# Optimization experiments

Hardware: AMD Instinct MI355X
Metric: run time of the kernel (lower is better)

Reference implementation:

```python
import jax, jax.numpy as jnp
import numpy as np
from functools import partial

# Gate order along axis 0 of Wi/bi/Wh/bh: 0=r (input gate), 1=f (forget), 2=g (cell), 3=o (output)

def setup_inputs() -> dict:
    key = jax.random.key(0)
    ks = jax.random.split(key, 6)
    B, T, V, E, H, O = 64, 512, 32000, 256, 512, 1
    s_e, s_h = 1.0 / np.sqrt(E), 1.0 / np.sqrt(H)
    return {
        "input_words": jax.random.randint(ks[0], (B, T), 0, V, dtype=jnp.int64),
        "emb": jax.random.normal(ks[1], (V, E), dtype=jnp.float32) * 0.02,
        "Wi": jax.random.normal(ks[2], (4, H, E), dtype=jnp.float32) * s_e,
        "bi": jnp.zeros((4, H), dtype=jnp.float32),
        "Wh": jax.random.normal(ks[3], (4, H, H), dtype=jnp.float32) * s_h,
        "bh": jnp.zeros((4, H), dtype=jnp.float32),
        "Wfc": jax.random.normal(ks[4], (O, H), dtype=jnp.float32) * s_h,
        "bfc": jnp.zeros((O,), dtype=jnp.float32),
    }


def reference(input_words, emb, Wi, bi, Wh, bh, Wfc, bfc):
    B, T = input_words.shape
    H = Wh.shape[-1]
    x = emb[input_words]                     # [B, T, E]
    # Precompute input projections for all 4 gates, all timesteps: one big GEMM.
    xg = jnp.einsum('bte,ghe->tbgh', x, Wi) + bi  # [T, B, 4, H]

    def step(carry, xg_t):
        h, c = carry
        gates = xg_t + jnp.einsum('bk,ghk->bgh', h, Wh) + bh  # [B, 4, H]
        r = jax.nn.sigmoid(gates[:, 0])
        f = jax.nn.sigmoid(gates[:, 1])
        g = jnp.tanh(gates[:, 2])
        o = jax.nn.sigmoid(gates[:, 3])
        c = f * c + r * g
        h = o * jnp.tanh(c)
        return (h, c), None

    h0 = jnp.zeros((B, H), dtype=x.dtype)
    c0 = jnp.zeros((B, H), dtype=x.dtype)
    (h, c), _ = jax.lax.scan(step, (h0, c0), xg)
    out = jax.nn.sigmoid(h @ Wfc.T + bfc)    # [B, n_output]
    return (out, h)
```

## Files before the change

kernel.cpp:

```cpp
#include <hip/hip_runtime.h>
#include <hip/hip_bf16.h>

#define TB 512
#define NB 64
#define EE 256
#define HH 512
#define ND 8
#define DB 8
#define NBLK 8
#define NT 256
#define NCOLP 260
#define NPAIR 256
#define GCOLS 2048
#define SLOWOFF ((size_t)0x40000)
#define XGOFF   ((size_t)1 << 20)

typedef __bf16 bf16_t;
typedef bf16_t bf16x8 __attribute__((ext_vector_type(8)));
typedef float  f32x4  __attribute__((ext_vector_type(4)));
typedef unsigned u32;
typedef unsigned long long u64;
typedef u32 u32x4 __attribute__((ext_vector_type(4)));

__device__ __forceinline__ float sigf(float x) { return 1.0f / (1.0f + __expf(-x)); }
__device__ __forceinline__ float tanhfast(float x) {
    float xc = fminf(fmaxf(x, -15.0f), 15.0f);
    float e  = __expf(2.0f * xc);
    return (e - 1.0f) / (e + 1.0f);
}
__device__ __forceinline__ u32 bfbits(float f) {
    bf16_t h = (bf16_t)f;
    return (u32)__builtin_bit_cast(unsigned short, h);
}
__device__ __forceinline__ bf16x8 cvt8(float4 a, float4 b) {
    bf16x8 v;
    v[0]=(bf16_t)a.x; v[1]=(bf16_t)a.y; v[2]=(bf16_t)a.z; v[3]=(bf16_t)a.w;
    v[4]=(bf16_t)b.x; v[5]=(bf16_t)b.y; v[6]=(bf16_t)b.z; v[7]=(bf16_t)b.w;
    return v;
}
__device__ __forceinline__ f32x4 cvtxg(u64 v) {
    f32x4 r;
    r[0] = __uint_as_float((u32)( v        & 0xFFFFu) << 16);
    r[1] = __uint_as_float((u32)((v >> 16) & 0xFFFFu) << 16);
    r[2] = __uint_as_float((u32)((v >> 32) & 0xFFFFu) << 16);
    r[3] = __uint_as_float((u32)((v >> 48) & 0xFFFFu) << 16);
    return r;
}

__device__ __forceinline__ void bar_lds() {
    __builtin_amdgcn_sched_barrier(0);
    asm volatile("s_waitcnt lgkmcnt(0)" ::: "memory");
    __builtin_amdgcn_s_barrier();
    __builtin_amdgcn_sched_barrier(0);
}

__device__ __forceinline__ void poll8_dual(const u64* fsrc, const u64* ssrc,
                                           u32 tag, u64 (&pk)[4]) {
    u64 fa = (u64)fsrc;
    int it = 0;
    for (;;) {
        u32x4 q0, q1, q2, q3;
        asm volatile(
            "global_load_dwordx4 %0, %4, off sc0\n\t"
            "global_load_dwordx4 %1, %4, off offset:16 sc0\n\t"
            "global_load_dwordx4 %2, %4, off offset:32 sc0\n\t"
            "global_load_dwordx4 %3, %4, off offset:48 sc0\n\t"
            "s_waitcnt vmcnt(0)"
            : "=&v"(q0), "=&v"(q1), "=&v"(q2), "=&v"(q3)
            : "v"(fa)
            : "memory");
        if (q0[1]==tag && q0[3]==tag && q1[1]==tag && q1[3]==tag &&
            q2[1]==tag && q2[3]==tag && q3[1]==tag && q3[3]==tag) {
            pk[0] = (u64)q0[0] | ((u64)q0[2] << 32);
            pk[1] = (u64)q1[0] | ((u64)q1[2] << 32);
            pk[2] = (u64)q2[0] | ((u64)q2[2] << 32);
            pk[3] = (u64)q3[0] | ((u64)q3[2] << 32);
            return;
        }
        if (((++it) & 7) == 0) {
            u64 hv[8];
            #pragma unroll
            for (int j = 0; j < 8; ++j)
                hv[j] = __hip_atomic_load(ssrc + j, __ATOMIC_RELAXED, __HIP_MEMORY_SCOPE_AGENT);
            bool ok = true;
            #pragma unroll
            for (int j = 0; j < 8; ++j) ok &= ((u32)(hv[j] >> 32) == tag);
            if (ok) {
                #pragma unroll
                for (int k = 0; k < 4; ++k)
                    pk[k] = (u64)(u32)hv[2*k] | ((u64)(u32)hv[2*k + 1] << 32);
                return;
            }
        }
    }
}

__global__ __launch_bounds__(256, 1)
void xg_prepass(const int* __restrict__ words, const float* __restrict__ emb,
                const float* __restrict__ Wi, const float* __restrict__ bi,
                const float* __restrict__ bh, bf16_t* __restrict__ xgT)
{
    const int tid = threadIdx.x, lane = tid & 63, wv = tid >> 6;
    const int kgrp = lane >> 4, cl = lane & 15;
    const int cc = blockIdx.x & 7, tc = blockIdx.x >> 3;

    __shared__ __align__(16) bf16_t x_s[64][EE];

    bf16x8 wf[8][4];
    float  bv[4];
    #pragma unroll
    for (int nt = 0; nt < 4; ++nt) {
        int col = cc*256 + wv*64 + nt*16 + cl;
        int wrow = (col & 3)*HH + (col >> 2);
        const float* wr = Wi + (size_t)wrow*EE;
        #pragma unroll
        for (int kt = 0; kt < 8; ++kt) {
            const float4* p = (const float4*)(wr + kt*32 + kgrp*8);
            wf[kt][nt] = cvt8(p[0], p[1]);
        }
        bv[nt] = bi[wrow] + bh[wrow];
    }

    const int r0 = tid >> 2, q = tid & 3;
    const int swz = (r0 & 7) << 3;
    u64* dst = (u64*)xgT;

    for (int it = 0; it < 16; ++it) {
        int t = tc*16 + it;
        {
            int wd = words[r0*TB + t];
            const float4* p = (const float4*)(emb + (size_t)wd*EE + q*64);
            #pragma unroll
            for (int o = 0; o < 8; ++o) {
                float4 a = p[2*o], b2 = p[2*o + 1];
                *(bf16x8*)&x_s[r0][(q*64 + o*8) ^ swz] = cvt8(a, b2);
            }
        }
        __syncthreads();

        f32x4 acc[4][4];
        #pragma unroll
        for (int rt = 0; rt < 4; ++rt)
            #pragma unroll
            for (int nt = 0; nt < 4; ++nt)
                acc[rt][nt] = (f32x4){ bv[nt], bv[nt], bv[nt], bv[nt] };
        #pragma unroll
        for (int kt = 0; kt < 8; ++kt) {
            #pragma unroll
            for (int rt = 0; rt < 4; ++rt) {
                bf16x8 a = *(const bf16x8*)&x_s[rt*16 + cl][(kt*32 + kgrp*8) ^ ((cl & 7) << 3)];
                #pragma unroll
                for (int nt = 0; nt < 4; ++nt)
                    acc[rt][nt] = __builtin_amdgcn_mfma_f32_16x16x32_bf16(a, wf[kt][nt], acc[rt][nt], 0, 0, 0);
            }
        }
        #pragma unroll
        for (int nt = 0; nt < 4; ++nt) {
            int col = cc*256 + wv*64 + nt*16 + cl;
            #pragma unroll
            for (int rt = 0; rt < 4; ++rt) {
                f32x4 v = acc[rt][nt];
                u64 pkk =  (u64)(bfbits(v[0]))
                        | ((u64)(bfbits(v[1])) << 16)
                        | ((u64)(bfbits(v[2])) << 32)
                        | ((u64)(bfbits(v[3])) << 48);
                dst[(size_t)(t*GCOLS + col)*16 + rt*4 + kgrp] = pkk;
            }
        }
        __syncthreads();
    }
}

__global__ __launch_bounds__(NT, 1)
void lstm_main(const float* __restrict__ Wh,
               const float* __restrict__ Wfc,
               const float* __restrict__ bfc,
               float* __restrict__ out,
               u64* __restrict__ fastH,
               u64* __restrict__ slowH,
               const u64* __restrict__ xg64)
{
    const int tid  = threadIdx.x;
    const int lane = tid & 63;
    const int wv   = tid >> 6;
    const int g    = blockIdx.x & 7;
    const int ug   = blockIdx.x >> 3;
    const int kgrp = lane >> 4;
    const int cl   = lane & 15;

    __shared__ __align__(16) bf16_t h_lds[16][HH];
    __shared__ __align__(16) float  P_lds[16][NCOLP];

    for (int i = tid; i < 16*HH/2; i += NT) ((u32*)h_lds)[i] = 0u;

    bf16x8 whf[16][4];
    #pragma unroll
    for (int nt = 0; nt < 4; ++nt) {
        int gc = ug*256 + wv*64 + nt*16 + cl;
        int wrow = (gc & 3)*HH + (gc >> 2);
        const float* wr = Wh + (size_t)wrow*HH;
        #pragma unroll
        for (int kt = 0; kt < 16; ++kt) {
            const float4* p = (const float4*)(wr + kt*32 + kgrp*8);
            whf[kt][nt] = cvt8(p[0], p[1]);
        }
    }

    const int sb = tid >> 5, sc = tid & 31;
    const int swz = sb << 3;

    const bool xlive = (kgrp < 2);
    const int m = 2*g + kgrp;
    int gc[4];
    #pragma unroll
    for (int nt = 0; nt < 4; ++nt) gc[nt] = ug*256 + wv*64 + nt*16 + cl;

    u64 xgc[4] = {0,0,0,0}, xgn[4] = {0,0,0,0};
    if (xlive) {
        #pragma unroll
        for (int nt = 0; nt < 4; ++nt) xgc[nt] = xg64[(size_t)gc[nt]*16 + m];
    }

    float c0 = 0.f, c1 = 0.f;
    __syncthreads();

    for (int t = 0; t < TB; ++t) {
        if (t > 0) {
            size_t off = ((size_t)((t & 1) ^ 1))*NB*NPAIR
                       + (size_t)(g*DB + sb)*NPAIR + sc*8;
            u64 pk[4];
            poll8_dual(fastH + off, slowH + off, (u32)t, pk);
            #pragma unroll
            for (int k = 0; k < 4; ++k) {
                int e = sc*16 + 4*k;
                int phys = ((e & ~7) ^ swz) | (e & 7);
                *(u64*)&h_lds[sb][phys] = pk[k];
            }
        }

        if (xlive && t + 1 < TB) {
            #pragma unroll
            for (int nt = 0; nt < 4; ++nt)
                xgn[nt] = xg64[(size_t)((t + 1)*GCOLS + gc[nt])*16 + m];
        }
        bar_lds();

        f32x4 acc[4];
        #pragma unroll
        for (int nt = 0; nt < 4; ++nt)
            acc[nt] = xlive ? cvtxg(xgc[nt]) : (f32x4){0.f,0.f,0.f,0.f};
        if (t > 0) {
            #pragma unroll
            for (int kt = 0; kt < 16; ++kt) {
                bf16x8 a = *(const bf16x8*)&h_lds[cl][(kt*32 + kgrp*8) ^ ((cl & 7) << 3)];
                #pragma unroll
                for (int nt = 0; nt < 4; ++nt)
                    acc[nt] = __builtin_amdgcn_mfma_f32_16x16x32_bf16(a, whf[kt][nt], acc[nt], 0, 0, 0);
            }
        }

        if (xlive) {
            #pragma unroll
            for (int nt = 0; nt < 4; ++nt)
                #pragma unroll
                for (int r = 0; r < 4; ++r)
                    P_lds[kgrp*4 + r][wv*64 + nt*16 + cl] = acc[nt][r];
        }
        bar_lds();

        {
            float4 g0 = *(const float4*)&P_lds[sb][sc*8];
            float4 g1 = *(const float4*)&P_lds[sb][sc*8 + 4];
            float r0 = sigf(g0.x), f0 = sigf(g0.y), z0 = tanhfast(g0.z), o0 = sigf(g0.w);
            float r1 = sigf(g1.x), f1 = sigf(g1.y), z1 = tanhfast(g1.z), o1 = sigf(g1.w);
            c0 = f0*c0 + r0*z0;
            c1 = f1*c1 + r1*z1;
            float h0 = o0*tanhfast(c0);
            float h1 = o1*tanhfast(c1);
            if (t == TB - 1) {
                float2 hw = { h0, h1 };
                *(float2*)&out[64 + (size_t)(g*DB + sb)*HH + ug*64 + 2*sc] = hw;
            }
            u64 v = (((u64)(u32)(t + 1)) << 32)
                  | (u64)(bfbits(h0) | (bfbits(h1) << 16));
            size_t di = ((size_t)(t & 1))*NB*NPAIR
                      + (size_t)(g*DB + sb)*NPAIR + ug*32 + sc;
            asm volatile("global_store_dwordx2 %0, %1, off sc0"
                         :: "v"((u64)(fastH + di)), "v"(v) : "memory");
            __hip_atomic_store(slowH + di, v, __ATOMIC_RELAXED, __HIP_MEMORY_SCOPE_AGENT);
        }
        #pragma unroll
        for (int nt = 0; nt < 4; ++nt) xgc[nt] = xgn[nt];
    }

    if (ug == 0) {
        size_t off = ((size_t)((TB - 1) & 1))*NB*NPAIR
                   + (size_t)(g*DB + sb)*NPAIR + sc*8;
        u64 pk[4];
        poll8_dual(fastH + off, slowH + off, (u32)TB, pk);
        float s = 0.f;
        const float4* wp = (const float4*)(Wfc + sc*16);
        #pragma unroll
        for (int k = 0; k < 4; ++k) {
            float4 w = wp[k];
            u64 p = pk[k];
            s += __uint_as_float((u32)( p        & 0xFFFFu) << 16) * w.x;
            s += __uint_as_float((u32)((p >> 16) & 0xFFFFu) << 16) * w.y;
            s += __uint_as_float((u32)((p >> 32) & 0xFFFFu) << 16) * w.z;
            s += __uint_as_float((u32)((p >> 48) & 0xFFFFu) << 16) * w.w;
        }
        __syncthreads();
        P_lds[sb][sc] = s;
        __syncthreads();
        if (tid < 8) {
            float acc = 0.f;
            #pragma unroll
            for (int q = 0; q < 32; ++q) acc += P_lds[tid][q];
            out[g*DB + tid] = sigf(acc + bfc[0]);
        }
    }
}

extern "C" void kernel_launch(void* const* d_in, const int* in_sizes, int n_in,
                              void* d_out, int out_size, void* d_ws, size_t ws_size,
                              hipStream_t stream) {
    (void)in_sizes; (void)n_in; (void)out_size; (void)ws_size;
    const int*   words = (const int*)d_in[0];
    const float* emb   = (const float*)d_in[1];
    const float* Wi    = (const float*)d_in[2];
    const float* bi    = (const float*)d_in[3];
    const float* Wh    = (const float*)d_in[4];
    const float* bh    = (const float*)d_in[5];
    const float* Wfc   = (const float*)d_in[6];
    const float* bfc   = (const float*)d_in[7];
    float* out = (float*)d_out;

    u64* fastH  = (u64*)d_ws;
    u64* slowH  = (u64*)((char*)d_ws + SLOWOFF);
    bf16_t* xgT = (bf16_t*)((char*)d_ws + XGOFF);

    hipMemsetAsync(d_ws, 0, 2*SLOWOFF, stream);

    xg_prepass<<<dim3(256), dim3(256), 0, stream>>>(words, emb, Wi, bi, bh, xgT);
    lstm_main<<<dim3(ND*NBLK), dim3(NT), 0, stream>>>(Wh, Wfc, bfc, out,
                                                      fastH, slowH, (const u64*)xgT);
}
```

Before: 2.213 ms.

## Add dedicated publisher wave that batches hidden-state stores to global memory

Adds a fifth wavefront per block that collects the freshly computed hidden values from shared memory and writes them to the fast and slow exchange buffers in batched 4-wide stores, instead of every compute thread issuing its own store pair. Compute waves now stage h into an LDS buffer, and an extra barrier is added per timestep. It also makes the slow-path poll fallback run every 4 iterations instead of 8. The aim is to reduce store instruction count on the critical cross-block handoff, at the cost of an extra barrier and one more wave per block.

```diff
diff --git a/kernel.cpp b/kernel.cpp
--- a/kernel.cpp
+++ b/kernel.cpp
@@ -8,7 +8,8 @@
 #define ND 8
 #define DB 8
 #define NBLK 8
-#define NT 256
+#define NT 320
+#define NC 256
 #define NCOLP 260
 #define NPAIR 256
 #define GCOLS 2048
@@ -77,7 +78,7 @@
             pk[3] = (u64)q3[0] | ((u64)q3[2] << 32);
             return;
         }
-        if (((++it) & 7) == 0) {
+        if (((++it) & 3) == 0) {
             u64 hv[8];
             #pragma unroll
             for (int j = 0; j < 8; ++j)
@@ -187,45 +188,51 @@
     const int ug   = blockIdx.x >> 3;
     const int kgrp = lane >> 4;
     const int cl   = lane & 15;
+    const bool cw  = (tid < NC);
 
     __shared__ __align__(16) bf16_t h_lds[16][HH];
     __shared__ __align__(16) float  P_lds[16][NCOLP];
+    __shared__ __align__(16) u64    h_out[8][32];
 
     for (int i = tid; i < 16*HH/2; i += NT) ((u32*)h_lds)[i] = 0u;
 
     bf16x8 whf[16][4];
-    #pragma unroll
-    for (int nt = 0; nt < 4; ++nt) {
-        int gc = ug*256 + wv*64 + nt*16 + cl;
-        int wrow = (gc & 3)*HH + (gc >> 2);
-        const float* wr = Wh + (size_t)wrow*HH;
-        #pragma unroll
-        for (int kt = 0; kt < 16; ++kt) {
-            const float4* p = (const float4*)(wr + kt*32 + kgrp*8);
-            whf[kt][nt] = cvt8(p[0], p[1]);
+    if (cw) {
+        #pragma unroll
+        for (int nt = 0; nt < 4; ++nt) {
+            int gc = ug*256 + wv*64 + nt*16 + cl;
+            int wrow = (gc & 3)*HH + (gc >> 2);
+            const float* wr = Wh + (size_t)wrow*HH;
+            #pragma unroll
+            for (int kt = 0; kt < 16; ++kt) {
+                const float4* p = (const float4*)(wr + kt*32 + kgrp*8);
+                whf[kt][nt] = cvt8(p[0], p[1]);
+            }
         }
     }
 
     const int sb = tid >> 5, sc = tid & 31;
-    const int swz = sb << 3;
-
-    const bool xlive = (kgrp < 2);
-    const int m = 2*g + kgrp;
+    const int swz = (sb & 7) << 3;
+
+    const int m = 2*g + (kgrp & 1);
     int gc[4];
     #pragma unroll
     for (int nt = 0; nt < 4; ++nt) gc[nt] = ug*256 + wv*64 + nt*16 + cl;
 
     u64 xgc[4] = {0,0,0,0}, xgn[4] = {0,0,0,0};
-    if (xlive) {
+    if (cw) {
         #pragma unroll
         for (int nt = 0; nt < 4; ++nt) xgc[nt] = xg64[(size_t)gc[nt]*16 + m];
     }
+
+    const int ml = tid - NC;
+    const int mb = ml >> 3, mj = ml & 7;
 
     float c0 = 0.f, c1 = 0.f;
     __syncthreads();
 
     for (int t = 0; t < TB; ++t) {
-        if (t > 0) {
+        if (cw && t > 0) {
             size_t off = ((size_t)((t & 1) ^ 1))*NB*NPAIR
                        + (size_t)(g*DB + sb)*NPAIR + sc*8;
             u64 pk[4];
@@ -238,28 +245,26 @@
             }
         }
 
-        if (xlive && t + 1 < TB) {
+        if (cw && t + 1 < TB) {
             #pragma unroll
             for (int nt = 0; nt < 4; ++nt)
                 xgn[nt] = xg64[(size_t)((t + 1)*GCOLS + gc[nt])*16 + m];
         }
         bar_lds();
 
-        f32x4 acc[4];
-        #pragma unroll
-        for (int nt = 0; nt < 4; ++nt)
-            acc[nt] = xlive ? cvtxg(xgc[nt]) : (f32x4){0.f,0.f,0.f,0.f};
-        if (t > 0) {
-            #pragma unroll
-            for (int kt = 0; kt < 16; ++kt) {
-                bf16x8 a = *(const bf16x8*)&h_lds[cl][(kt*32 + kgrp*8) ^ ((cl & 7) << 3)];
+        if (cw) {
+            f32x4 acc[4];
+            #pragma unroll
+            for (int nt = 0; nt < 4; ++nt) acc[nt] = cvtxg(xgc[nt]);
+            if (t > 0) {
                 #pragma unroll
-                for (int nt = 0; nt < 4; ++nt)
-                    acc[nt] = __builtin_amdgcn_mfma_f32_16x16x32_bf16(a, whf[kt][nt], acc[nt], 0, 0, 0);
-            }
-        }
-
-        if (xlive) {
+                for (int kt = 0; kt < 16; ++kt) {
+                    bf16x8 a = *(const bf16x8*)&h_lds[cl][(kt*32 + kgrp*8) ^ ((cl & 7) << 3)];
+                    #pragma unroll
+                    for (int nt = 0; nt < 4; ++nt)
+                        acc[nt] = __builtin_amdgcn_mfma_f32_16x16x32_bf16(a, whf[kt][nt], acc[nt], 0, 0, 0);
+                }
+            }
             #pragma unroll
             for (int nt = 0; nt < 4; ++nt)
                 #pragma unroll
@@ -268,7 +273,7 @@
         }
         bar_lds();
 
-        {
+        if (cw) {
             float4 g0 = *(const float4*)&P_lds[sb][sc*8];
             float4 g1 = *(const float4*)&P_lds[sb][sc*8 + 4];
             float r0 = sigf(g0.x), f0 = sigf(g0.y), z0 = tanhfast(g0.z), o0 = sigf(g0.w);
@@ -281,36 +286,56 @@
                 float2 hw = { h0, h1 };
                 *(float2*)&out[64 + (size_t)(g*DB + sb)*HH + ug*64 + 2*sc] = hw;
             }
-            u64 v = (((u64)(u32)(t + 1)) << 32)
-                  | (u64)(bfbits(h0) | (bfbits(h1) << 16));
+            h_out[sb][sc] = (((u64)(u32)(t + 1)) << 32)
+                          | (u64)(bfbits(h0) | (bfbits(h1) << 16));
+        }
+        bar_lds();
+
+        if (!cw) {
+            u64 v0 = h_out[mb][mj*4 + 0];
+            u64 v1 = h_out[mb][mj*4 + 1];
+            u64 v2 = h_out[mb][mj*4 + 2];
+            u64 v3 = h_out[mb][mj*4 + 3];
             size_t di = ((size_t)(t & 1))*NB*NPAIR
-                      + (size_t)(g*DB + sb)*NPAIR + ug*32 + sc;
-            asm volatile("global_store_dwordx2 %0, %1, off sc0"
-                         :: "v"((u64)(fastH + di)), "v"(v) : "memory");
-            __hip_atomic_store(slowH + di, v, __ATOMIC_RELAXED, __HIP_MEMORY_SCOPE_AGENT);
-        }
-        #pragma unroll
-        for (int nt = 0; nt < 4; ++nt) xgc[nt] = xgn[nt];
+                      + (size_t)(g*DB + mb)*NPAIR + ug*32 + mj*4;
+            u64 fa = (u64)(fastH + di);
+            asm volatile(
+                "global_store_dwordx2 %0, %1, off sc0\n\t"
+                "global_store_dwordx2 %0, %2, off offset:8 sc0\n\t"
+                "global_store_dwordx2 %0, %3, off offset:16 sc0\n\t"
+                "global_store_dwordx2 %0, %4, off offset:24 sc0"
+                :: "v"(fa), "v"(v0), "v"(v1), "v"(v2), "v"(v3) : "memory");
+            __hip_atomic_store(slowH + di + 0, v0, __ATOMIC_RELAXED, __HIP_MEMORY_SCOPE_AGENT);
+            __hip_atomic_store(slowH + di + 1, v1, __ATOMIC_RELAXED, __HIP_MEMORY_SCOPE_AGENT);
+            __hip_atomic_store(slowH + di + 2, v2, __ATOMIC_RELAXED, __HIP_MEMORY_SCOPE_AGENT);
+            __hip_atomic_store(slowH + di + 3, v3, __ATOMIC_RELAXED, __HIP_MEMORY_SCOPE_AGENT);
+        }
+        if (cw) {
+            #pragma unroll
+            for (int nt = 0; nt < 4; ++nt) xgc[nt] = xgn[nt];
+        }
     }
 
     if (ug == 0) {
-        size_t off = ((size_t)((TB - 1) & 1))*NB*NPAIR
-                   + (size_t)(g*DB + sb)*NPAIR + sc*8;
-        u64 pk[4];
-        poll8_dual(fastH + off, slowH + off, (u32)TB, pk);
         float s = 0.f;
-        const float4* wp = (const float4*)(Wfc + sc*16);
-        #pragma unroll
-        for (int k = 0; k < 4; ++k) {
-            float4 w = wp[k];
-            u64 p = pk[k];
-            s += __uint_as_float((u32)( p        & 0xFFFFu) << 16) * w.x;
-            s += __uint_as_float((u32)((p >> 16) & 0xFFFFu) << 16) * w.y;
-            s += __uint_as_float((u32)((p >> 32) & 0xFFFFu) << 16) * w.z;
-            s += __uint_as_float((u32)((p >> 48) & 0xFFFFu) << 16) * w.w;
+        if (cw) {
+            size_t off = ((size_t)((TB - 1) & 1))*NB*NPAIR
+                       + (size_t)(g*DB + sb)*NPAIR + sc*8;
+            u64 pk[4];
+            poll8_dual(fastH + off, slowH + off, (u32)TB, pk);
+            const float4* wp = (const float4*)(Wfc + sc*16);
+            #pragma unroll
+            for (int k = 0; k < 4; ++k) {
+                float4 w = wp[k];
+                u64 p = pk[k];
+                s += __uint_as_float((u32)( p        & 0xFFFFu) << 16) * w.x;
+                s += __uint_as_float((u32)((p >> 16) & 0xFFFFu) << 16) * w.y;
+                s += __uint_as_float((u32)((p >> 32) & 0xFFFFu) << 16) * w.z;
+                s += __uint_as_float((u32)((p >> 48) & 0xFFFFu) << 16) * w.w;
+            }
         }
         __syncthreads();
-        P_lds[sb][sc] = s;
+        if (cw) P_lds[sb][sc] = s;
         __syncthreads();
         if (tid < 8) {
             float acc = 0.f;
```

New measurement: 2.963 ms. 1.34x slower.
